# Kernel optimization log

Measured on AMD Instinct MI355X. Metric: run time of the kernel, lower is better.

The kernel has to match this reference:

```python
import jax, jax.numpy as jnp
import numpy as np

H = 0.1  # spatial delta h from init kwargs


def _stencils():
    k_avg = jnp.array([[0., 0., 0.], [0., 1., 0.], [0., 0., 0.]], jnp.float32)
    k_x = (0.5 / H) * jnp.array([[0., -1., 0.], [0., 0., 0.], [0., 1., 0.]], jnp.float32)
    k_y = (0.5 / H) * jnp.array([[0., 0., 0.], [-1., 0., 1.], [0., 0., 0.]], jnp.float32)
    k_xx = (1.0 / H ** 2) * jnp.array([[0., 1., 0.], [0., -2., 0.], [0., 1., 0.]], jnp.float32)
    k_yy = (1.0 / H ** 2) * jnp.array([[0., 0., 0.], [1., -2., 1.], [0., 0., 0.]], jnp.float32)
    return k_avg, k_x, k_y, k_xx, k_yy


def setup_inputs() -> dict:
    key = jax.random.key(0)
    ks = jax.random.split(key, 11)
    B = 65536
    inp = {
        'data': jax.random.normal(ks[0], (B, 3, 11, 11), jnp.float32),
        'mix_a': jax.random.normal(ks[1], (128, 5 * 3 * 81), jnp.float32),
        'mix_b': jax.random.normal(ks[2], (128,), jnp.float32),
        'w1': jax.random.normal(ks[3], (128, 128), jnp.float32) * 0.08,
        'b1': jax.random.normal(ks[4], (128,), jnp.float32) * 0.05,
        'w2': jax.random.normal(ks[5], (128, 128), jnp.float32) * 0.08,
        'b2': jax.random.normal(ks[6], (128,), jnp.float32) * 0.05,
        'w3': jax.random.normal(ks[7], (128, 128), jnp.float32) * 0.08,
        'b3': jax.random.normal(ks[8], (128,), jnp.float32) * 0.05,
        'wf': jax.random.normal(ks[9], (5, 128), jnp.float32) * 0.08,
        'bf': jax.random.normal(ks[10], (5,), jnp.float32) * 0.05,
    }
    return inp


def reference(data, mix_a, mix_b, w1, b1, w2, b2, w3, b3, wf, bf):
    b = data.shape[0]
    # 3x3 patches over the 11x11 grid -> (b, c, 3, 3, 9, 9); last two dims are the
    # 9x9 valid output positions (l = n*9+m, matching torch unfold's reshape order).
    patches = jnp.stack(
        [jnp.stack([data[:, :, i:i + 9, j:j + 9] for j in range(3)], axis=2)
         for i in range(3)], axis=2)
    feats = [jnp.einsum('bcijnm,ij->bcnm', patches, k).reshape(b, -1)
             for k in _stencils()]  # each (b, 3*81)
    mixed = jnp.concatenate(feats, axis=1) @ mix_a.T + mix_b  # (b, 128)
    x = jnp.tanh(mixed)
    x = jnp.tanh(x @ w1.T + b1)
    x = jnp.tanh(x @ w2.T + b2)
    x = jnp.tanh(x @ w3.T + b3)
    return x @ wf.T + bf  # (b, 5)
```

## Files before the change

### kernel.cpp

```cpp
#include <hip/hip_runtime.h>
#include <hip/hip_bf16.h>

typedef __attribute__((ext_vector_type(4))) float f32x4;
typedef __attribute__((ext_vector_type(8))) short bf16x8;

#define MFMA(a,b,c) __builtin_amdgcn_mfma_f32_16x16x32_bf16((a),(b),(c),0,0,0)

__device__ inline void split_bf16(float a, unsigned short &h, unsigned short &l) {
    unsigned u = __float_as_uint(a);
    unsigned rh = (u + 0x7FFFu + ((u >> 16) & 1u)) & 0xFFFF0000u;
    float hf = __uint_as_float(rh);
    h = (unsigned short)(rh >> 16);
    float lf = a - hf;
    unsigned u2 = __float_as_uint(lf);
    l = (unsigned short)((u2 + 0x7FFFu + ((u2 >> 16) & 1u)) >> 16);
}

__device__ inline float tanh_fast(float x) {
    float e = __expf(2.f * x);
    return 1.f - 2.f * __builtin_amdgcn_rcpf(e + 1.f);
}

__global__ void prep_weff(const float* __restrict__ mix_a,
                          unsigned short* __restrict__ wph,
                          unsigned short* __restrict__ wpl) {
    int idx = blockIdx.x * 256 + threadIdx.x;
    if (idx >= 128 * 384) return;
    int o = idx / 384;
    int k = idx - o * 384;
    float acc = 0.f;
    if (k < 363) {
        int c = k / 121, rem = k - c * 121;
        int y = rem / 11, x = rem - y * 11;
        const float* ma = mix_a + (size_t)o * 1215 + c * 81;
        auto add = [&](int f, int i, int j, float coef) {
            int n = y - i, m = x - j;
            if (n >= 0 && n < 9 && m >= 0 && m < 9)
                acc += ma[f * 243 + n * 9 + m] * coef;
        };
        add(0, 1, 1, 1.f);
        add(1, 0, 1, -5.f);  add(1, 2, 1, 5.f);
        add(2, 1, 0, -5.f);  add(2, 1, 2, 5.f);
        add(3, 0, 1, 100.f); add(3, 1, 1, -200.f); add(3, 2, 1, 100.f);
        add(4, 1, 0, 100.f); add(4, 1, 1, -200.f); add(4, 1, 2, 100.f);
    }
    unsigned short h, l; split_bf16(acc, h, l);
    int kt = k >> 5, ot = o >> 4;
    int lane = (o & 15) + 16 * ((k >> 3) & 3);
    int jj = k & 7;
    int pidx = ((kt * 8 + ot) * 64 + lane) * 8 + jj;
    wph[pidx] = h; wpl[pidx] = l;
}

__global__ void prep_layers(const float* __restrict__ w1, const float* __restrict__ w2,
                            const float* __restrict__ w3, const float* __restrict__ wf,
                            unsigned short* __restrict__ wlh, unsigned short* __restrict__ wll,
                            unsigned short* __restrict__ wfh, unsigned short* __restrict__ wfl) {
    int idx = blockIdx.x * 256 + threadIdx.x;
    if (idx < 3 * 16384) {
        int layer = idx >> 14; int rem = idx & 16383;
        int o = rem >> 7, k = rem & 127;
        const float* w = (layer == 0) ? w1 : ((layer == 1) ? w2 : w3);
        float v = w[o * 128 + k];
        unsigned short h, l; split_bf16(v, h, l);
        int kt = k >> 5, ot = o >> 4;
        int lane = (o & 15) + 16 * ((k >> 3) & 3);
        int pidx = layer * 16384 + ((kt * 8 + ot) * 64 + lane) * 8 + (k & 7);
        wlh[pidx] = h; wll[pidx] = l;
    } else if (idx < 3 * 16384 + 2048) {
        int rem = idx - 3 * 16384;
        int o = rem >> 7, k = rem & 127;
        float v = (o < 5) ? wf[o * 128 + k] : 0.f;
        unsigned short h, l; split_bf16(v, h, l);
        int kt = k >> 5;
        int lane = (o & 15) + 16 * ((k >> 3) & 3);
        int pidx = (kt * 64 + lane) * 8 + (k & 7);
        wfh[pidx] = h; wfl[pidx] = l;
    }
}

__global__ __launch_bounds__(256, 2)
void fused_main(const float* __restrict__ data,
                const float* __restrict__ mix_b,
                const float* __restrict__ b1v,
                const float* __restrict__ b2v,
                const float* __restrict__ b3v,
                const float* __restrict__ bfv,
                const unsigned short* __restrict__ wp1h,
                const unsigned short* __restrict__ wp1l,
                const unsigned short* __restrict__ wlh,
                const unsigned short* __restrict__ wll,
                const unsigned short* __restrict__ wfh,
                const unsigned short* __restrict__ wfl,
                float* __restrict__ out, int Btot) {
    __shared__ __align__(16) unsigned short XsH[4][2][16][136];
    __shared__ __align__(16) unsigned short XsL[4][2][16][136];

    const int wave = threadIdx.x >> 6;
    const int lane = threadIdx.x & 63;
    const int s0 = (blockIdx.x * 4 + wave) * 32;
    if (s0 >= Btot) return;
    const int col = lane & 15;
    const int kg  = lane >> 4;

    const float* ap0 = data + (size_t)(s0 + col) * 363;
    const float* ap1 = ap0 + (size_t)16 * 363;

    f32x4 acc[2][8];
    #pragma unroll
    for (int ot = 0; ot < 8; ++ot) {
        float b = mix_b[col + 16 * ot];
        acc[0][ot] = (f32x4){b, b, b, b};
        acc[1][ot] = (f32x4){b, b, b, b};
    }

    float abuf[2][2][16];
    #pragma unroll
    for (int kt = 0; kt < 2; ++kt)
        #pragma unroll
        for (int j = 0; j < 8; ++j) {
            int k = kt * 32 + kg * 8 + j;
            abuf[0][0][kt * 8 + j] = ap0[k];
            abuf[0][1][kt * 8 + j] = ap1[k];
        }

    #pragma unroll
    for (int c = 0; c < 6; ++c) {
        const int kc = c * 64;
        const int cur = c & 1, nxt = cur ^ 1;
        if (c < 5) {
            #pragma unroll
            for (int kt = 0; kt < 2; ++kt)
                #pragma unroll
                for (int j = 0; j < 8; ++j) {
                    int k = kc + 64 + kt * 32 + kg * 8 + j;
                    bool ok = (k < 363);
                    abuf[nxt][0][kt * 8 + j] = ok ? ap0[k] : 0.f;
                    abuf[nxt][1][kt * 8 + j] = ok ? ap1[k] : 0.f;
                }
        }
        #pragma unroll
        for (int kt = 0; kt < 2; ++kt) {
            bf16x8 ah[2], al[2];
            #pragma unroll
            for (int t = 0; t < 2; ++t)
                #pragma unroll
                for (int j = 0; j < 8; ++j) {
                    unsigned short h, l;
                    split_bf16(abuf[cur][t][kt * 8 + j], h, l);
                    ah[t][j] = (short)h; al[t][j] = (short)l;
                }
            const int ktg = kc / 32 + kt;
            const unsigned short* ph = wp1h + ((size_t)(ktg * 8) * 64 + (size_t)lane) * 8;
            const unsigned short* pl = wp1l + ((size_t)(ktg * 8) * 64 + (size_t)lane) * 8;
            #pragma unroll
            for (int ot = 0; ot < 8; ++ot) {
                bf16x8 bh = *(const bf16x8*)(ph + (size_t)ot * 512);
                bf16x8 bl = *(const bf16x8*)(pl + (size_t)ot * 512);
                acc[0][ot] = MFMA(ah[0], bh, acc[0][ot]);
                acc[0][ot] = MFMA(ah[0], bl, acc[0][ot]);
                acc[0][ot] = MFMA(al[0], bh, acc[0][ot]);
                acc[1][ot] = MFMA(ah[1], bh, acc[1][ot]);
                acc[1][ot] = MFMA(ah[1], bl, acc[1][ot]);
                acc[1][ot] = MFMA(al[1], bh, acc[1][ot]);
            }
        }
    }

    #pragma unroll
    for (int t = 0; t < 2; ++t)
        #pragma unroll
        for (int ot = 0; ot < 8; ++ot)
            #pragma unroll
            for (int j = 0; j < 4; ++j) {
                float x = tanh_fast(acc[t][ot][j]);
                unsigned short h, l; split_bf16(x, h, l);
                XsH[wave][t][kg * 4 + j][col + 16 * ot] = h;
                XsL[wave][t][kg * 4 + j][col + 16 * ot] = l;
            }

    const float* biases[3] = {b1v, b2v, b3v};
    #pragma unroll
    for (int layer = 0; layer < 3; ++layer) {
        asm volatile("s_waitcnt lgkmcnt(0)" ::: "memory");
        const float* bb = biases[layer];
        f32x4 nacc[2][8];
        #pragma unroll
        for (int ot = 0; ot < 8; ++ot) {
            float b = bb[col + 16 * ot];
            nacc[0][ot] = (f32x4){b, b, b, b};
            nacc[1][ot] = (f32x4){b, b, b, b};
        }
        const unsigned short* ph0 = wlh + (size_t)layer * 16384;
        const unsigned short* pl0 = wll + (size_t)layer * 16384;
        #pragma unroll
        for (int kt = 0; kt < 4; ++kt) {
            bf16x8 xh[2], xl[2];
            #pragma unroll
            for (int t = 0; t < 2; ++t) {
                xh[t] = *(const bf16x8*)&XsH[wave][t][col][kt * 32 + kg * 8];
                xl[t] = *(const bf16x8*)&XsL[wave][t][col][kt * 32 + kg * 8];
            }
            #pragma unroll
            for (int ot = 0; ot < 8; ++ot) {
                bf16x8 bh = *(const bf16x8*)(ph0 + ((size_t)(kt * 8 + ot) * 64 + lane) * 8);
                bf16x8 bl = *(const bf16x8*)(pl0 + ((size_t)(kt * 8 + ot) * 64 + lane) * 8);
                nacc[0][ot] = MFMA(xh[0], bh, nacc[0][ot]);
                nacc[0][ot] = MFMA(xh[0], bl, nacc[0][ot]);
                nacc[0][ot] = MFMA(xl[0], bh, nacc[0][ot]);
                nacc[1][ot] = MFMA(xh[1], bh, nacc[1][ot]);
                nacc[1][ot] = MFMA(xh[1], bl, nacc[1][ot]);
                nacc[1][ot] = MFMA(xl[1], bh, nacc[1][ot]);
            }
        }
        asm volatile("s_waitcnt lgkmcnt(0)" ::: "memory");
        #pragma unroll
        for (int t = 0; t < 2; ++t)
            #pragma unroll
            for (int ot = 0; ot < 8; ++ot)
                #pragma unroll
                for (int j = 0; j < 4; ++j) {
                    float x = tanh_fast(nacc[t][ot][j]);
                    unsigned short h, l; split_bf16(x, h, l);
                    XsH[wave][t][kg * 4 + j][col + 16 * ot] = h;
                    XsL[wave][t][kg * 4 + j][col + 16 * ot] = l;
                }
    }

    asm volatile("s_waitcnt lgkmcnt(0)" ::: "memory");
    float fb = (col < 5) ? bfv[col] : 0.f;
    f32x4 facc[2];
    facc[0] = (f32x4){fb, fb, fb, fb};
    facc[1] = (f32x4){fb, fb, fb, fb};
    #pragma unroll
    for (int kt = 0; kt < 4; ++kt) {
        bf16x8 bh = *(const bf16x8*)(wfh + ((size_t)kt * 64 + lane) * 8);
        bf16x8 bl = *(const bf16x8*)(wfl + ((size_t)kt * 64 + lane) * 8);
        #pragma unroll
        for (int t = 0; t < 2; ++t) {
            bf16x8 xh = *(const bf16x8*)&XsH[wave][t][col][kt * 32 + kg * 8];
            bf16x8 xl = *(const bf16x8*)&XsL[wave][t][col][kt * 32 + kg * 8];
            facc[t] = MFMA(xh, bh, facc[t]);
            facc[t] = MFMA(xh, bl, facc[t]);
            facc[t] = MFMA(xl, bh, facc[t]);
        }
    }
    if (col < 5) {
        #pragma unroll
        for (int t = 0; t < 2; ++t)
            #pragma unroll
            for (int j = 0; j < 4; ++j) {
                int s = s0 + 16 * t + kg * 4 + j;
                if (s < Btot) out[(size_t)s * 5 + col] = facc[t][j];
            }
    }
}

extern "C" void kernel_launch(void* const* d_in, const int* in_sizes, int n_in,
                              void* d_out, int out_size, void* d_ws, size_t ws_size,
                              hipStream_t stream) {
    const float* data  = (const float*)d_in[0];
    const float* mix_a = (const float*)d_in[1];
    const float* mix_b = (const float*)d_in[2];
    const float* w1    = (const float*)d_in[3];
    const float* b1    = (const float*)d_in[4];
    const float* w2    = (const float*)d_in[5];
    const float* b2    = (const float*)d_in[6];
    const float* w3    = (const float*)d_in[7];
    const float* b3    = (const float*)d_in[8];
    const float* wf    = (const float*)d_in[9];
    const float* bf    = (const float*)d_in[10];
    float* out = (float*)d_out;
    int Btot = in_sizes[0] / 363;

    if (ws_size < 401408) return;
    unsigned short* wp1h = (unsigned short*)d_ws;
    unsigned short* wp1l = wp1h + 49152;
    unsigned short* wlh  = wp1l + 49152;
    unsigned short* wll  = wlh + 49152;
    unsigned short* wfh  = wll + 49152;
    unsigned short* wfl  = wfh + 2048;

    prep_weff<<<192, 256, 0, stream>>>(mix_a, wp1h, wp1l);
    prep_layers<<<200, 256, 0, stream>>>(w1, w2, w3, wf, wlh, wll, wfh, wfl);
    int blocks = (Btot + 127) / 128;
    fused_main<<<blocks, 256, 0, stream>>>(data, mix_b, b1, b2, b3, bf,
                                           wp1h, wp1l, wlh, wll, wfh, wfl, out, Btot);
}
```

Measured before the change: 219.6 us.

## Software-pipeline weight and input loads across k-steps and merge prep kernels

Merges the two weight-prep kernels into one launch. In the main fused kernel, the per-k-step stage now double-buffers the high bf16 weight fragments one step ahead and loads the input rows as 16-byte vectors instead of scalar loads. The MFMAs are regrouped so each split term (hh, lh, hl) is issued across all output tiles in sequence. The hidden layers apply the same prefetch of the next high weights across layer boundaries. The aim is to hide global weight-load latency behind MFMA work and cut a launch, at the cost of more VGPRs, which may lower occupancy.

```diff
diff --git a/kernel.cpp b/kernel.cpp
--- a/kernel.cpp
+++ b/kernel.cpp
@@ -21,42 +21,43 @@
     return 1.f - 2.f * __builtin_amdgcn_rcpf(e + 1.f);
 }
 
-__global__ void prep_weff(const float* __restrict__ mix_a,
-                          unsigned short* __restrict__ wph,
-                          unsigned short* __restrict__ wpl) {
+__device__ inline bf16x8 ldb(const unsigned short* p) { return *(const bf16x8*)p; }
+__device__ inline f32x4 ld4u(const float* p) { f32x4 v; __builtin_memcpy(&v, p, 16); return v; }
+
+__global__ void prep_all(const float* __restrict__ mix_a,
+                         const float* __restrict__ w1, const float* __restrict__ w2,
+                         const float* __restrict__ w3, const float* __restrict__ wf,
+                         unsigned short* __restrict__ wph, unsigned short* __restrict__ wpl,
+                         unsigned short* __restrict__ wlh, unsigned short* __restrict__ wll,
+                         unsigned short* __restrict__ wfh, unsigned short* __restrict__ wfl) {
     int idx = blockIdx.x * 256 + threadIdx.x;
-    if (idx >= 128 * 384) return;
-    int o = idx / 384;
-    int k = idx - o * 384;
-    float acc = 0.f;
-    if (k < 363) {
-        int c = k / 121, rem = k - c * 121;
-        int y = rem / 11, x = rem - y * 11;
-        const float* ma = mix_a + (size_t)o * 1215 + c * 81;
-        auto add = [&](int f, int i, int j, float coef) {
-            int n = y - i, m = x - j;
-            if (n >= 0 && n < 9 && m >= 0 && m < 9)
-                acc += ma[f * 243 + n * 9 + m] * coef;
-        };
-        add(0, 1, 1, 1.f);
-        add(1, 0, 1, -5.f);  add(1, 2, 1, 5.f);
-        add(2, 1, 0, -5.f);  add(2, 1, 2, 5.f);
-        add(3, 0, 1, 100.f); add(3, 1, 1, -200.f); add(3, 2, 1, 100.f);
-        add(4, 1, 0, 100.f); add(4, 1, 1, -200.f); add(4, 1, 2, 100.f);
-    }
-    unsigned short h, l; split_bf16(acc, h, l);
-    int kt = k >> 5, ot = o >> 4;
-    int lane = (o & 15) + 16 * ((k >> 3) & 3);
-    int jj = k & 7;
-    int pidx = ((kt * 8 + ot) * 64 + lane) * 8 + jj;
-    wph[pidx] = h; wpl[pidx] = l;
-}
-
-__global__ void prep_layers(const float* __restrict__ w1, const float* __restrict__ w2,
-                            const float* __restrict__ w3, const float* __restrict__ wf,
-                            unsigned short* __restrict__ wlh, unsigned short* __restrict__ wll,
-                            unsigned short* __restrict__ wfh, unsigned short* __restrict__ wfl) {
-    int idx = blockIdx.x * 256 + threadIdx.x;
+    if (idx < 128 * 384) {
+        int o = idx / 384;
+        int k = idx - o * 384;
+        float acc = 0.f;
+        if (k < 363) {
+            int c = k / 121, rem = k - c * 121;
+            int y = rem / 11, x = rem - y * 11;
+            const float* ma = mix_a + (size_t)o * 1215 + c * 81;
+            auto add = [&](int f, int i, int j, float coef) {
+                int n = y - i, m = x - j;
+                if (n >= 0 && n < 9 && m >= 0 && m < 9)
+                    acc += ma[f * 243 + n * 9 + m] * coef;
+            };
+            add(0, 1, 1, 1.f);
+            add(1, 0, 1, -5.f);  add(1, 2, 1, 5.f);
+            add(2, 1, 0, -5.f);  add(2, 1, 2, 5.f);
+            add(3, 0, 1, 100.f); add(3, 1, 1, -200.f); add(3, 2, 1, 100.f);
+            add(4, 1, 0, 100.f); add(4, 1, 1, -200.f); add(4, 1, 2, 100.f);
+        }
+        unsigned short h, l; split_bf16(acc, h, l);
+        int kt = k >> 5, ot = o >> 4;
+        int lane = (o & 15) + 16 * ((k >> 3) & 3);
+        int pidx = ((kt * 8 + ot) * 64 + lane) * 8 + (k & 7);
+        wph[pidx] = h; wpl[pidx] = l;
+        return;
+    }
+    idx -= 128 * 384;
     if (idx < 3 * 16384) {
         int layer = idx >> 14; int rem = idx & 16383;
         int o = rem >> 7, k = rem & 127;
@@ -103,8 +104,8 @@
     const int col = lane & 15;
     const int kg  = lane >> 4;
 
-    const float* ap0 = data + (size_t)(s0 + col) * 363;
-    const float* ap1 = ap0 + (size_t)16 * 363;
+    const float* arow0 = data + (size_t)(s0 + col) * 363;
+    const float* arow1 = arow0 + (size_t)16 * 363;
 
     f32x4 acc[2][8];
     #pragma unroll
@@ -114,56 +115,66 @@
         acc[1][ot] = (f32x4){b, b, b, b};
     }
 
-    float abuf[2][2][16];
-    #pragma unroll
-    for (int kt = 0; kt < 2; ++kt)
-        #pragma unroll
-        for (int j = 0; j < 8; ++j) {
-            int k = kt * 32 + kg * 8 + j;
-            abuf[0][0][kt * 8 + j] = ap0[k];
-            abuf[0][1][kt * 8 + j] = ap1[k];
-        }
-
-    #pragma unroll
-    for (int c = 0; c < 6; ++c) {
-        const int kc = c * 64;
-        const int cur = c & 1, nxt = cur ^ 1;
-        if (c < 5) {
-            #pragma unroll
-            for (int kt = 0; kt < 2; ++kt)
+    bf16x8 bh[2][8], bl[8];
+    f32x4 a4[2][2][2];
+    a4[0][0][0] = ld4u(arow0 + kg * 8);     a4[0][0][1] = ld4u(arow0 + kg * 8 + 4);
+    a4[0][1][0] = ld4u(arow1 + kg * 8);     a4[0][1][1] = ld4u(arow1 + kg * 8 + 4);
+    #pragma unroll
+    for (int ot = 0; ot < 8; ++ot)
+        bh[0][ot] = ldb(wp1h + ((size_t)ot * 64 + lane) * 8);
+
+    #pragma unroll
+    for (int ktg = 0; ktg < 12; ++ktg) {
+        const int p = ktg & 1;
+        #pragma unroll
+        for (int ot = 0; ot < 8; ++ot)
+            bl[ot] = ldb(wp1l + (((size_t)(ktg * 8 + ot)) * 64 + lane) * 8);
+        if (ktg < 11) {
+            #pragma unroll
+            for (int ot = 0; ot < 8; ++ot)
+                bh[p ^ 1][ot] = ldb(wp1h + (((size_t)((ktg + 1) * 8 + ot)) * 64 + lane) * 8);
+        }
+        if (ktg < 10) {
+            const int kb = (ktg + 1) * 32 + kg * 8;
+            a4[p ^ 1][0][0] = ld4u(arow0 + kb); a4[p ^ 1][0][1] = ld4u(arow0 + kb + 4);
+            a4[p ^ 1][1][0] = ld4u(arow1 + kb); a4[p ^ 1][1][1] = ld4u(arow1 + kb + 4);
+        } else if (ktg == 10) {
+            #pragma unroll
+            for (int i = 0; i < 2; ++i)
                 #pragma unroll
-                for (int j = 0; j < 8; ++j) {
-                    int k = kc + 64 + kt * 32 + kg * 8 + j;
+                for (int j = 0; j < 4; ++j) {
+                    int k = 352 + kg * 8 + i * 4 + j;
                     bool ok = (k < 363);
-                    abuf[nxt][0][kt * 8 + j] = ok ? ap0[k] : 0.f;
-                    abuf[nxt][1][kt * 8 + j] = ok ? ap1[k] : 0.f;
+                    a4[p ^ 1][0][i][j] = ok ? arow0[k] : 0.f;
+                    a4[p ^ 1][1][i][j] = ok ? arow1[k] : 0.f;
                 }
         }
-        #pragma unroll
-        for (int kt = 0; kt < 2; ++kt) {
-            bf16x8 ah[2], al[2];
-            #pragma unroll
-            for (int t = 0; t < 2; ++t)
+        bf16x8 ah[2], al[2];
+        #pragma unroll
+        for (int t = 0; t < 2; ++t)
+            #pragma unroll
+            for (int i = 0; i < 2; ++i)
                 #pragma unroll
-                for (int j = 0; j < 8; ++j) {
-                    unsigned short h, l;
-                    split_bf16(abuf[cur][t][kt * 8 + j], h, l);
-                    ah[t][j] = (short)h; al[t][j] = (short)l;
+                for (int j = 0; j < 4; ++j) {
+                    unsigned short hh, ll;
+                    split_bf16(a4[p][t][i][j], hh, ll);
+                    ah[t][i * 4 + j] = (short)hh;
+                    al[t][i * 4 + j] = (short)ll;
                 }
-            const int ktg = kc / 32 + kt;
-            const unsigned short* ph = wp1h + ((size_t)(ktg * 8) * 64 + (size_t)lane) * 8;
-            const unsigned short* pl = wp1l + ((size_t)(ktg * 8) * 64 + (size_t)lane) * 8;
-            #pragma unroll
-            for (int ot = 0; ot < 8; ++ot) {
-                bf16x8 bh = *(const bf16x8*)(ph + (size_t)ot * 512);
-                bf16x8 bl = *(const bf16x8*)(pl + (size_t)ot * 512);
-                acc[0][ot] = MFMA(ah[0], bh, acc[0][ot]);
-                acc[0][ot] = MFMA(ah[0], bl, acc[0][ot]);
-                acc[0][ot] = MFMA(al[0], bh, acc[0][ot]);
-                acc[1][ot] = MFMA(ah[1], bh, acc[1][ot]);
-                acc[1][ot] = MFMA(ah[1], bl, acc[1][ot]);
-                acc[1][ot] = MFMA(al[1], bh, acc[1][ot]);
-            }
+        #pragma unroll
+        for (int ot = 0; ot < 8; ++ot) {
+            acc[0][ot] = MFMA(ah[0], bh[p][ot], acc[0][ot]);
+            acc[1][ot] = MFMA(ah[1], bh[p][ot], acc[1][ot]);
+        }
+        #pragma unroll
+        for (int ot = 0; ot < 8; ++ot) {
+            acc[0][ot] = MFMA(al[0], bh[p][ot], acc[0][ot]);
+            acc[1][ot] = MFMA(al[1], bh[p][ot], acc[1][ot]);
+        }
+        #pragma unroll
+        for (int ot = 0; ot < 8; ++ot) {
+            acc[0][ot] = MFMA(ah[0], bl[ot], acc[0][ot]);
+            acc[1][ot] = MFMA(ah[1], bl[ot], acc[1][ot]);
         }
     }
 
@@ -180,9 +191,14 @@
             }
 
     const float* biases[3] = {b1v, b2v, b3v};
+    bf16x8 lbh[2][8], lbl[8];
+    asm volatile("s_waitcnt lgkmcnt(0)" ::: "memory");
+    #pragma unroll
+    for (int ot = 0; ot < 8; ++ot)
+        lbh[0][ot] = ldb(wlh + ((size_t)ot * 64 + lane) * 8);
+
     #pragma unroll
     for (int layer = 0; layer < 3; ++layer) {
-        asm volatile("s_waitcnt lgkmcnt(0)" ::: "memory");
         const float* bb = biases[layer];
         f32x4 nacc[2][8];
         #pragma unroll
@@ -191,10 +207,21 @@
             nacc[0][ot] = (f32x4){b, b, b, b};
             nacc[1][ot] = (f32x4){b, b, b, b};
         }
-        const unsigned short* ph0 = wlh + (size_t)layer * 16384;
         const unsigned short* pl0 = wll + (size_t)layer * 16384;
         #pragma unroll
         for (int kt = 0; kt < 4; ++kt) {
+            const int s = layer * 4 + kt;
+            const int p = s & 1;
+            #pragma unroll
+            for (int ot = 0; ot < 8; ++ot)
+                lbl[ot] = ldb(pl0 + (((size_t)(kt * 8 + ot)) * 64 + lane) * 8);
+            if (s < 11) {
+                const int nl = (s + 1) >> 2, nk = (s + 1) & 3;
+                const unsigned short* ph = wlh + (size_t)nl * 16384;
+                #pragma unroll
+                for (int ot = 0; ot < 8; ++ot)
+                    lbh[p ^ 1][ot] = ldb(ph + (((size_t)(nk * 8 + ot)) * 64 + lane) * 8);
+            }
             bf16x8 xh[2], xl[2];
             #pragma unroll
             for (int t = 0; t < 2; ++t) {
@@ -203,14 +230,18 @@
             }
             #pragma unroll
             for (int ot = 0; ot < 8; ++ot) {
-                bf16x8 bh = *(const bf16x8*)(ph0 + ((size_t)(kt * 8 + ot) * 64 + lane) * 8);
-                bf16x8 bl = *(const bf16x8*)(pl0 + ((size_t)(kt * 8 + ot) * 64 + lane) * 8);
-                nacc[0][ot] = MFMA(xh[0], bh, nacc[0][ot]);
-                nacc[0][ot] = MFMA(xh[0], bl, nacc[0][ot]);
-                nacc[0][ot] = MFMA(xl[0], bh, nacc[0][ot]);
-                nacc[1][ot] = MFMA(xh[1], bh, nacc[1][ot]);
-                nacc[1][ot] = MFMA(xh[1], bl, nacc[1][ot]);
-                nacc[1][ot] = MFMA(xl[1], bh, nacc[1][ot]);
+                nacc[0][ot] = MFMA(xh[0], lbh[p][ot], nacc[0][ot]);
+                nacc[1][ot] = MFMA(xh[1], lbh[p][ot], nacc[1][ot]);
+            }
+            #pragma unroll
+            for (int ot = 0; ot < 8; ++ot) {
+                nacc[0][ot] = MFMA(xl[0], lbh[p][ot], nacc[0][ot]);
+                nacc[1][ot] = MFMA(xl[1], lbh[p][ot], nacc[1][ot]);
+            }
+            #pragma unroll
+            for (int ot = 0; ot < 8; ++ot) {
+                nacc[0][ot] = MFMA(xh[0], lbl[ot], nacc[0][ot]);
+                nacc[1][ot] = MFMA(xh[1], lbl[ot], nacc[1][ot]);
             }
         }
         asm volatile("s_waitcnt lgkmcnt(0)" ::: "memory");
@@ -225,24 +256,24 @@
                     XsH[wave][t][kg * 4 + j][col + 16 * ot] = h;
                     XsL[wave][t][kg * 4 + j][col + 16 * ot] = l;
                 }
-    }
-
-    asm volatile("s_waitcnt lgkmcnt(0)" ::: "memory");
+        asm volatile("s_waitcnt lgkmcnt(0)" ::: "memory");
+    }
+
     float fb = (col < 5) ? bfv[col] : 0.f;
     f32x4 facc[2];
     facc[0] = (f32x4){fb, fb, fb, fb};
     facc[1] = (f32x4){fb, fb, fb, fb};
     #pragma unroll
     for (int kt = 0; kt < 4; ++kt) {
-        bf16x8 bh = *(const bf16x8*)(wfh + ((size_t)kt * 64 + lane) * 8);
-        bf16x8 bl = *(const bf16x8*)(wfl + ((size_t)kt * 64 + lane) * 8);
+        bf16x8 fh = ldb(wfh + ((size_t)kt * 64 + lane) * 8);
+        bf16x8 fl = ldb(wfl + ((size_t)kt * 64 + lane) * 8);
         #pragma unroll
         for (int t = 0; t < 2; ++t) {
             bf16x8 xh = *(const bf16x8*)&XsH[wave][t][col][kt * 32 + kg * 8];
             bf16x8 xl = *(const bf16x8*)&XsL[wave][t][col][kt * 32 + kg * 8];
-            facc[t] = MFMA(xh, bh, facc[t]);
-            facc[t] = MFMA(xh, bl, facc[t]);
-            facc[t] = MFMA(xl, bh, facc[t]);
+            facc[t] = MFMA(xh, fh, facc[t]);
+            facc[t] = MFMA(xl, fh, facc[t]);
+            facc[t] = MFMA(xh, fl, facc[t]);
         }
     }
     if (col < 5) {
@@ -281,8 +312,8 @@
     unsigned short* wfh  = wll + 49152;
     unsigned short* wfl  = wfh + 2048;
 
-    prep_weff<<<192, 256, 0, stream>>>(mix_a, wp1h, wp1l);
-    prep_layers<<<200, 256, 0, stream>>>(w1, w2, w3, wf, wlh, wll, wfh, wfl);
+    prep_all<<<392, 256, 0, stream>>>(mix_a, w1, w2, w3, wf,
+                                      wp1h, wp1l, wlh, wll, wfh, wfl);
     int blocks = (Btot + 127) / 128;
     fused_main<<<blocks, 256, 0, stream>>>(data, mix_b, b1, b2, b3, bf,
                                            wp1h, wp1l, wlh, wll, wfh, wfl, out, Btot);
```

After: 207.0 us. 1.06x faster.
